# Kernel optimization log

Hardware: AMD Instinct MI355X
Metric: run time of the kernel (lower is better)

Reference implementation:

```python
import jax, jax.numpy as jnp
import numpy as np

B, N, C = 2, 2048, 1024
H = 16
D = C // H  # 64
EPS = 1e-6


def rms_norm(x, w):
    # LlamaRMSNorm: fp32 variance over last dim
    xf = x.astype(jnp.float32)
    var = jnp.mean(xf * xf, axis=-1, keepdims=True)
    xf = xf * jax.lax.rsqrt(var + EPS)
    return (w * xf).astype(x.dtype)


def setup_inputs() -> dict:
    key = jax.random.key(0)
    ks = jax.random.split(key, 4)
    x = jax.random.normal(ks[0], (B, N, C), dtype=jnp.float32)
    mask = jax.random.randint(ks[1], (B, N), 0, 2, dtype=jnp.int32)
    qkv_w = jax.random.normal(ks[2], (3 * C, C), dtype=jnp.float32) * (1.0 / np.sqrt(C))
    qkv_b = jnp.zeros((3 * C,), dtype=jnp.float32)
    proj_w = jax.random.normal(ks[3], (C, C), dtype=jnp.float32) * (1.0 / np.sqrt(C))
    proj_b = jnp.zeros((C,), dtype=jnp.float32)
    qn_w = jnp.ones((D,), dtype=jnp.float32)
    kn_w = jnp.ones((D,), dtype=jnp.float32)
    return {"x": x, "mask": mask, "qkv_w": qkv_w, "qkv_b": qkv_b,
            "proj_w": proj_w, "proj_b": proj_b, "qn_w": qn_w, "kn_w": kn_w}


def reference(x, mask, qkv_w, qkv_b, proj_w, proj_b, qn_w, kn_w):
    dtype = x.dtype
    scale = D ** -0.5
    # qkv projection -> (3, B, H, N, D)
    qkv = (x @ qkv_w.T + qkv_b).reshape(B, N, 3, H, D).transpose(2, 0, 3, 1, 4)
    q, k, v = qkv[0], qkv[1], qkv[2]
    q = rms_norm(q, qn_w)
    k = rms_norm(k, kn_w)
    q = q * scale
    # scores in fp32, key-padding mask [B,1,1,N]
    attn = jnp.einsum('bhnd,bhmd->bhnm', q, k).astype(jnp.float32)
    key_mask = (mask != 0)[:, None, None, :]
    attn = jnp.where(key_mask, attn, jnp.float32(-1e9))
    attn = jax.nn.softmax(attn, axis=-1).astype(dtype)
    out = jnp.einsum('bhnm,bhmd->bhnd', attn, v)  # (B,H,N,D)
    out = out.transpose(0, 2, 1, 3).reshape(B, N, C)
    return out @ proj_w.T + proj_b
```

## Files before the change

kernel.cpp:

```cpp
#include <hip/hip_runtime.h>
#include <hip/hip_bf16.h>
#include <stdint.h>

namespace {

constexpr int kB = 2;
constexpr int kN = 2048;
constexpr int kC = 1024;
constexpr int kH = 16;
constexpr int kD = 64;
constexpr int kTok = kB * kN;
constexpr int k3C  = 3 * kC;
constexpr size_t kPS = (size_t)kTok * k3C;
constexpr size_t kXE = (size_t)kTok * kC;
constexpr size_t kWQ = (size_t)k3C * kC;
constexpr size_t kWP = (size_t)kC * kC;

using bhalf8 = __attribute__((ext_vector_type(8))) __bf16;
using f32x4  = __attribute__((ext_vector_type(4))) float;

__device__ inline unsigned short f2bf(float f) {
  __hip_bfloat16 h = __float2bfloat16(f);
  return *reinterpret_cast<unsigned short*>(&h);
}
__device__ inline float bf2f(unsigned short u) {
  __hip_bfloat16 h;
  *reinterpret_cast<unsigned short*>(&h) = u;
  return __bfloat162float(h);
}
__device__ inline void split2(float v, unsigned short& h, unsigned short& l) {
  const unsigned short hb = f2bf(v);
  h = hb;
  l = f2bf(v - bf2f(hb));
}

__device__ inline void glds16(const unsigned short* g, unsigned short* l) {
  __builtin_amdgcn_global_load_lds(
      (const __attribute__((address_space(1))) void*)g,
      (__attribute__((address_space(3))) void*)l, 16, 0, 0);
}

__global__ __launch_bounds__(256)
void split_planes(const float* __restrict__ src,
                  unsigned short* __restrict__ H,
                  unsigned short* __restrict__ L, int n4)
{
  const int i = blockIdx.x * 256 + threadIdx.x;
  if (i >= n4) return;
  const float4 v = ((const float4*)src)[i];
  ushort4 hh, ll;
  split2(v.x, hh.x, ll.x); split2(v.y, hh.y, ll.y);
  split2(v.z, hh.z, ll.z); split2(v.w, hh.w, ll.w);
  ((ushort4*)H)[i] = hh;
  ((ushort4*)L)[i] = ll;
}

__global__ __launch_bounds__(256)
void vt_transpose(const unsigned short* __restrict__ H,
                  unsigned short* __restrict__ VTH)
{
  const int gw   = blockIdx.x * 4 + (threadIdx.x >> 6);
  const int lane = threadIdx.x & 63;
  const int bh   = gw >> 8;
  const int oct  = gw & 255;
  const int b = bh >> 4, h = bh & 15;
  const int tok0 = oct * 8;
  union { unsigned short u[8]; uint4 v; } ph;
  #pragma unroll
  for (int e = 0; e < 8; ++e) {
    const size_t g = (size_t)(b * kN + tok0 + e) * k3C + 2 * kC + h * kD + lane;
    ph.u[e] = H[g];
  }
  *(uint4*)(&VTH[((size_t)bh * kD + lane) * kN + tok0]) = ph.v;
}

__global__ __launch_bounds__(512)
void gemm_qkv256(const unsigned short* __restrict__ AH,
                 const unsigned short* __restrict__ AL,
                 const unsigned short* __restrict__ WH,
                 const unsigned short* __restrict__ WL,
                 const float* __restrict__ bias,
                 unsigned short* __restrict__ OutH,
                 unsigned short* __restrict__ OutL,
                 const float* __restrict__ qn,
                 const float* __restrict__ kn)
{
  constexpr int BK = 32;
  constexpr int NT = kC / BK;

  __shared__ __align__(16) unsigned short sA[2][2][256 * 32];
  __shared__ __align__(16) unsigned short sB[2][2][256 * 32];

  const int tt   = threadIdx.x;
  const int wave = tt >> 6;
  const int lane = tt & 63;
  const int quad = lane >> 4;
  const int l16  = lane & 15;
  const int bm = blockIdx.x * 256;
  const int bn = blockIdx.y * 256;
  const int wm = (wave >> 2) * 128;
  const int wn = (wave & 3) * 64;

  int srow[2], scol[2];
  #pragma unroll
  for (int r = 0; r < 2; ++r) {
    const int u = r * 512 + tt;
    srow[r] = u >> 2;
    scol[r] = ((u & 3) ^ ((srow[r] >> 1) & 3)) * 8;
  }

  auto stagePair = [&](int buf, int k0, int which) {
    const unsigned short* src = (which == 0) ? AH : (which == 1) ? AL
                              : (which == 2) ? WH : WL;
    const int base = (which < 2) ? bm : bn;
    unsigned short* dst = (which < 2) ? &sA[buf][which][0]
                                      : &sB[buf][which - 2][0];
    #pragma unroll
    for (int r = 0; r < 2; ++r) {
      glds16(&src[(size_t)(base + srow[r]) * kC + k0 + scol[r]],
             &dst[(r * 512 + tt) * 8]);
    }
  };

  f32x4 acc[8][4] = {};

  #pragma unroll
  for (int w = 0; w < 4; ++w) stagePair(0, 0, w);

  for (int t = 0; t < NT; ++t) {
    const int buf  = t & 1;
    const int nbuf = buf ^ 1;
    const int nk0  = (t + 1) * BK;
    bhalf8 bh_[4], bl_[4];

    #pragma unroll
    for (int p = 0; p < 4; ++p) {
      bhalf8 ah[2], al[2];
      if (p == 0) {
        if (t < NT - 1) {
          stagePair(nbuf, nk0, 0);
          asm volatile("s_waitcnt vmcnt(2)" ::: "memory");
        } else {
          asm volatile("s_waitcnt vmcnt(0)" ::: "memory");
        }
        __builtin_amdgcn_sched_barrier(0);
        asm volatile("s_barrier" ::: "memory");
        #pragma unroll
        for (int j = 0; j < 4; ++j) {
          const int row = wn + j * 16 + l16;
          const int off = row * 32 + ((quad ^ ((row >> 1) & 3)) * 8);
          bh_[j] = *(const bhalf8*)(&sB[buf][0][off]);
          bl_[j] = *(const bhalf8*)(&sB[buf][1][off]);
        }
        #pragma unroll
        for (int e = 0; e < 2; ++e) {
          const int row = wm + e * 16 + l16;
          const int off = row * 32 + ((quad ^ ((row >> 1) & 3)) * 8);
          ah[e] = *(const bhalf8*)(&sA[buf][0][off]);
          al[e] = *(const bhalf8*)(&sA[buf][1][off]);
        }
      } else {
        #pragma unroll
        for (int e = 0; e < 2; ++e) {
          const int row = wm + (2 * p + e) * 16 + l16;
          const int off = row * 32 + ((quad ^ ((row >> 1) & 3)) * 8);
          ah[e] = *(const bhalf8*)(&sA[buf][0][off]);
          al[e] = *(const bhalf8*)(&sA[buf][1][off]);
        }
        if (t < NT - 1) stagePair(nbuf, nk0, p);
        asm volatile("s_barrier" ::: "memory");
      }

      __builtin_amdgcn_s_setprio(1);
      #pragma unroll
      for (int e = 0; e < 2; ++e) {
        const int i = 2 * p + e;
        #pragma unroll
        for (int j = 0; j < 4; ++j) {
          f32x4 a = acc[i][j];
          a = __builtin_amdgcn_mfma_f32_16x16x32_bf16(ah[e], bh_[j], a, 0, 0, 0);
          a = __builtin_amdgcn_mfma_f32_16x16x32_bf16(ah[e], bl_[j], a, 0, 0, 0);
          a = __builtin_amdgcn_mfma_f32_16x16x32_bf16(al[e], bh_[j], a, 0, 0, 0);
          acc[i][j] = a;
        }
      }
      __builtin_amdgcn_s_setprio(0);
      asm volatile("s_barrier" ::: "memory");
    }
  }

  const int slice = bn >> 10;
  const bool writeL = (slice == 0);
  float bv[4], wv[4];
  #pragma unroll
  for (int j = 0; j < 4; ++j) {
    bv[j] = bias[bn + wn + j * 16 + l16];
    if (slice < 2) wv[j] = (slice ? kn : qn)[j * 16 + l16];
  }

  #pragma unroll
  for (int i = 0; i < 8; ++i) {
    float val[4][4];
    #pragma unroll
    for (int j = 0; j < 4; ++j)
      #pragma unroll
      for (int r = 0; r < 4; ++r)
        val[j][r] = acc[i][j][r] + bv[j];

    if (slice < 2) {
      #pragma unroll
      for (int r = 0; r < 4; ++r) {
        float ss = val[0][r] * val[0][r];
        #pragma unroll
        for (int j = 1; j < 4; ++j) ss += val[j][r] * val[j][r];
        #pragma unroll
        for (int d = 1; d < 16; d <<= 1) ss += __shfl_xor(ss, d, 64);
        float rinv = rsqrtf(ss * (1.0f / 64.0f) + 1e-6f);
        if (slice == 0) rinv *= 0.125f;
        #pragma unroll
        for (int j = 0; j < 4; ++j) val[j][r] = wv[j] * (val[j][r] * rinv);
      }
    }

    #pragma unroll
    for (int j = 0; j < 4; ++j) {
      const int n = bn + wn + j * 16 + l16;
      #pragma unroll
      for (int r = 0; r < 4; ++r) {
        const int m = bm + wm + i * 16 + quad * 4 + r;
        unsigned short hh, ll;
        split2(val[j][r], hh, ll);
        OutH[(size_t)m * k3C + n] = hh;
        if (writeL) OutL[(size_t)m * k3C + n] = ll;
      }
    }
  }
}

template<bool OUTF32, bool FUSE_NORM>
__global__ __launch_bounds__(256)
void gemm_planes(const unsigned short* __restrict__ AH,
                 const unsigned short* __restrict__ AL, int lda,
                 const unsigned short* __restrict__ WH,
                 const unsigned short* __restrict__ WL,
                 const float* __restrict__ bias,
                 float* __restrict__ OutF,
                 unsigned short* __restrict__ OutH,
                 unsigned short* __restrict__ OutL,
                 const float* __restrict__ qn,
                 const float* __restrict__ kn,
                 int Nn, int K)
{
  __shared__ __align__(16) unsigned short AsH[128 * 32], AsL[128 * 32];
  __shared__ __align__(16) unsigned short BsH[128 * 32], BsL[128 * 32];

  const int t    = threadIdx.x;
  const int wave = t >> 6;
  const int lane = t & 63;
  const int quad = lane >> 4;
  const int l16  = lane & 15;
  const int bm = blockIdx.x * 128;
  const int bn = blockIdx.y * 128;
  const int wm = (wave >> 1) * 64;
  const int wn = (wave & 1) * 64;

  f32x4 acc[4][4] = {};

  for (int k0 = 0; k0 < K; k0 += 32) {
    #pragma unroll
    for (int r = 0; r < 2; ++r) {
      const int c   = r * 256 + t;
      const int row = c >> 2;
      const int col = (c & 3) * 8;
      glds16(&AH[(size_t)(bm + row) * lda + k0 + col], &AsH[c * 8]);
      glds16(&AL[(size_t)(bm + row) * lda + k0 + col], &AsL[c * 8]);
      glds16(&WH[(size_t)(bn + row) * K + k0 + col], &BsH[c * 8]);
      glds16(&WL[(size_t)(bn + row) * K + k0 + col], &BsL[c * 8]);
    }
    __syncthreads();

    bhalf8 afh[4], afl[4], bgh[4], bgl[4];
    #pragma unroll
    for (int i = 0; i < 4; ++i) {
      afh[i] = *(const bhalf8*)(&AsH[(wm + i * 16 + l16) * 32 + quad * 8]);
      afl[i] = *(const bhalf8*)(&AsL[(wm + i * 16 + l16) * 32 + quad * 8]);
      bgh[i] = *(const bhalf8*)(&BsH[(wn + i * 16 + l16) * 32 + quad * 8]);
      bgl[i] = *(const bhalf8*)(&BsL[(wn + i * 16 + l16) * 32 + quad * 8]);
    }
    #pragma unroll
    for (int i = 0; i < 4; ++i)
      #pragma unroll
      for (int j = 0; j < 4; ++j) {
        f32x4 a = acc[i][j];
        a = __builtin_amdgcn_mfma_f32_16x16x32_bf16(afh[i], bgh[j], a, 0, 0, 0);
        a = __builtin_amdgcn_mfma_f32_16x16x32_bf16(afh[i], bgl[j], a, 0, 0, 0);
        a = __builtin_amdgcn_mfma_f32_16x16x32_bf16(afl[i], bgh[j], a, 0, 0, 0);
        acc[i][j] = a;
      }
    __syncthreads();
  }

  float bv[4], wv[4];
  const int slice = FUSE_NORM ? (bn >> 10) : 0;
  const bool writeL = !FUSE_NORM || slice == 0;
  #pragma unroll
  for (int j = 0; j < 4; ++j) {
    bv[j] = bias[bn + wn + j * 16 + l16];
    if (FUSE_NORM && slice < 2)
      wv[j] = (slice ? kn : qn)[j * 16 + l16];
  }

  #pragma unroll
  for (int i = 0; i < 4; ++i) {
    float val[4][4];
    #pragma unroll
    for (int j = 0; j < 4; ++j)
      #pragma unroll
      for (int r = 0; r < 4; ++r)
        val[j][r] = acc[i][j][r] + bv[j];

    if (FUSE_NORM && slice < 2) {
      #pragma unroll
      for (int r = 0; r < 4; ++r) {
        float ss = val[0][r] * val[0][r];
        #pragma unroll
        for (int j = 1; j < 4; ++j) ss += val[j][r] * val[j][r];
        #pragma unroll
        for (int d = 1; d < 16; d <<= 1) ss += __shfl_xor(ss, d, 64);
        float rinv = rsqrtf(ss * (1.0f / 64.0f) + 1e-6f);
        if (slice == 0) rinv *= 0.125f;
        #pragma unroll
        for (int j = 0; j < 4; ++j) val[j][r] = wv[j] * (val[j][r] * rinv);
      }
    }

    #pragma unroll
    for (int j = 0; j < 4; ++j) {
      const int n = bn + wn + j * 16 + l16;
      #pragma unroll
      for (int r = 0; r < 4; ++r) {
        const int m = bm + wm + i * 16 + quad * 4 + r;
        if (OUTF32) {
          OutF[(size_t)m * Nn + n] = val[j][r];
        } else {
          unsigned short hh, ll;
          split2(val[j][r], hh, ll);
          OutH[(size_t)m * Nn + n] = hh;
          if (writeL) OutL[(size_t)m * Nn + n] = ll;
        }
      }
    }
  }
}

__global__ __launch_bounds__(256)
void attn_kernel(unsigned short* __restrict__ H, unsigned short* __restrict__ L,
                 const unsigned short* __restrict__ VTH,
                 const int* __restrict__ mask)
{
  constexpr int P = 72;
  __shared__ __align__(16) unsigned short KtH[64 * P];
  __shared__ __align__(16) unsigned short VtH[64 * P];
  __shared__ __align__(16) unsigned short Pt[4][32 * P];

  const int t    = threadIdx.x;
  const int wave = t >> 6;
  const int lane = t & 63;
  const int quad = lane >> 4;
  const int l16  = lane & 15;

  const int lin  = blockIdx.x;
  const int xcd  = lin & 7;
  const int slot = lin >> 3;
  const int bh   = xcd + 8 * (slot >> 4);
  const int qblk = slot & 15;
  const int b  = bh >> 4;
  const int h  = bh & 15;
  const int q0 = qblk * 128 + wave * 32;

  const int row0 = t >> 3,         col0 = (t & 7) * 8;
  const int row1 = (256 + t) >> 3, col1 = ((256 + t) & 7) * 8;

  bhalf8 qfh[2][2], qfl[2][2];
  #pragma unroll
  for (int g = 0; g < 2; ++g) {
    const size_t qrow = (size_t)(b * kN + q0 + g * 16 + l16) * k3C + h * kD;
    qfh[g][0] = *(const bhalf8*)(&H[qrow + quad * 8]);
    qfh[g][1] = *(const bhalf8*)(&H[qrow + 32 + quad * 8]);
    qfl[g][0] = *(const bhalf8*)(&L[qrow + quad * 8]);
    qfl[g][1] = *(const bhalf8*)(&L[qrow + 32 + quad * 8]);
  }

  f32x4 acc_o[2][4] = {};
  float lpart[2][4] = {};

  uint4 sk0, sk1, sv0, sv1;
  int mcur[4], mnext[4];

  auto pref = [&](int kt) {
    sk0 = *(const uint4*)(&H[(size_t)(b * kN + kt + row0) * k3C + kC + h * kD + col0]);
    sk1 = *(const uint4*)(&H[(size_t)(b * kN + kt + row1) * k3C + kC + h * kD + col1]);
    sv0 = *(const uint4*)(&VTH[((size_t)bh * kD + row0) * kN + kt + col0]);
    sv1 = *(const uint4*)(&VTH[((size_t)bh * kD + row1) * kN + kt + col1]);
  };
  auto loadM = [&](int kt, int* m) {
    #pragma unroll
    for (int nt = 0; nt < 4; ++nt) m[nt] = mask[b * kN + kt + nt * 16 + l16];
  };

  pref(0);
  loadM(0, mcur);

  for (int i = 0; i < 32; ++i) {
    const int kt = i * 64;
    *(uint4*)(&KtH[row0 * P + col0]) = sk0;
    *(uint4*)(&KtH[row1 * P + col1]) = sk1;
    *(uint4*)(&VtH[row0 * P + col0]) = sv0;
    *(uint4*)(&VtH[row1 * P + col1]) = sv1;
    __syncthreads();

    if (i < 31) { pref(kt + 64); loadM(kt + 64, mnext); }

    #pragma unroll
    for (int nt = 0; nt < 4; ++nt) {
      const int kr = (nt * 16 + l16) * P + quad * 8;
      const bhalf8 kh0 = *(const bhalf8*)(&KtH[kr]);
      const bhalf8 kh1 = *(const bhalf8*)(&KtH[kr + 32]);
      const float flag = mcur[nt] ? 1.0f : 0.0f;
      #pragma unroll
      for (int g = 0; g < 2; ++g) {
        f32x4 s = {};
        s = __builtin_amdgcn_mfma_f32_16x16x32_bf16(qfh[g][0], kh0, s, 0, 0, 0);
        s = __builtin_amdgcn_mfma_f32_16x16x32_bf16(qfh[g][1], kh1, s, 0, 0, 0);
        s = __builtin_amdgcn_mfma_f32_16x16x32_bf16(qfl[g][0], kh0, s, 0, 0, 0);
        s = __builtin_amdgcn_mfma_f32_16x16x32_bf16(qfl[g][1], kh1, s, 0, 0, 0);
        #pragma unroll
        for (int r = 0; r < 4; ++r) {
          const float p = flag * __expf(s[r]);
          lpart[g][r] += p;
          Pt[wave][(g * 16 + quad * 4 + r) * P + nt * 16 + l16] = f2bf(p);
        }
      }
    }

    #pragma unroll
    for (int kk = 0; kk < 2; ++kk) {
      const bhalf8 pa0 = *(const bhalf8*)(&Pt[wave][l16 * P + kk * 32 + quad * 8]);
      const bhalf8 pa1 = *(const bhalf8*)(&Pt[wave][(16 + l16) * P + kk * 32 + quad * 8]);
      #pragma unroll
      for (int dt = 0; dt < 4; ++dt) {
        const bhalf8 vb = *(const bhalf8*)(&VtH[(dt * 16 + l16) * P + kk * 32 + quad * 8]);
        acc_o[0][dt] = __builtin_amdgcn_mfma_f32_16x16x32_bf16(pa0, vb, acc_o[0][dt], 0, 0, 0);
        acc_o[1][dt] = __builtin_amdgcn_mfma_f32_16x16x32_bf16(pa1, vb, acc_o[1][dt], 0, 0, 0);
      }
    }

    #pragma unroll
    for (int nt = 0; nt < 4; ++nt) mcur[nt] = mnext[nt];
    __syncthreads();
  }

  #pragma unroll
  for (int g = 0; g < 2; ++g)
    #pragma unroll
    for (int r = 0; r < 4; ++r) {
      float s = lpart[g][r];
      #pragma unroll
      for (int d = 1; d < 16; d <<= 1) s += __shfl_xor(s, d, 64);
      lpart[g][r] = s;
    }
  #pragma unroll
  for (int g = 0; g < 2; ++g)
    #pragma unroll
    for (int dt = 0; dt < 4; ++dt)
      #pragma unroll
      for (int r = 0; r < 4; ++r) {
        const int qrow = q0 + g * 16 + quad * 4 + r;
        const float inv = 1.0f / fmaxf(lpart[g][r], 1.0e-30f);
        const size_t off = (size_t)(b * kN + qrow) * k3C + h * kD + dt * 16 + l16;
        unsigned short hh, ll;
        split2(acc_o[g][dt][r] * inv, hh, ll);
        H[off] = hh; L[off] = ll;
      }
}

}

extern "C" void kernel_launch(void* const* d_in, const int* in_sizes, int n_in,
                              void* d_out, int out_size, void* d_ws, size_t ws_size,
                              hipStream_t stream)
{
  const float* x      = (const float*)d_in[0];
  const int*   maskp  = (const int*)d_in[1];
  const float* qkv_w  = (const float*)d_in[2];
  const float* qkv_b  = (const float*)d_in[3];
  const float* proj_w = (const float*)d_in[4];
  const float* proj_b = (const float*)d_in[5];
  const float* qn_w   = (const float*)d_in[6];
  const float* kn_w   = (const float*)d_in[7];
  float* out = (float*)d_out;

  unsigned short* qH = (unsigned short*)d_ws;
  unsigned short* qL = qH + kPS;
  unsigned short* R1 = qL + kPS;
  unsigned short* R2 = R1 + 2 * kXE;
  unsigned short* xH = R1,  *xL = R1 + kXE;
  unsigned short* VTH = R1;
  unsigned short* wqH = R2, *wqL = R2 + kWQ;
  unsigned short* wpH = R2, *wpL = R2 + kWP;

  split_planes<<<(int)(kXE / 4 / 256), 256, 0, stream>>>(x, xH, xL, (int)(kXE / 4));
  split_planes<<<(int)(kWQ / 4 / 256), 256, 0, stream>>>(qkv_w, wqH, wqL, (int)(kWQ / 4));

  gemm_qkv256<<<dim3(kTok / 256, k3C / 256), 512, 0, stream>>>(
      xH, xL, wqH, wqL, qkv_b, qH, qL, qn_w, kn_w);

  vt_transpose<<<2048, 256, 0, stream>>>(qH, VTH);
  split_planes<<<(int)(kWP / 4 / 256), 256, 0, stream>>>(proj_w, wpH, wpL, (int)(kWP / 4));

  attn_kernel<<<dim3(512), 256, 0, stream>>>(qH, qL, VTH, maskp);

  gemm_planes<true, false><<<dim3(kTok / 128, kC / 128), 256, 0, stream>>>(
      qH, qL, k3C, wpH, wpL, proj_b, out, nullptr, nullptr, nullptr, nullptr, kC, kC);
}
```

Baseline: 311.4 us.

## Restructure split-bf16 GEMM main loop into plane-ordered phases with finer-grained staging

Reorganizes the QKV GEMM inner loop so each k-tile is processed as three phases (AH*WH, AH*WL, AL*WH), loading the LDS planes in the order they are consumed. Global-to-LDS staging for the next tile is interleaved per plane with partial vmcnt waits, and the last iteration is peeled. The aim is better overlap of memory traffic with MFMA work and fewer barriers per tile. In exchange it keeps more fragments live in registers (8 A fragments), which may raise register pressure and lower occupancy.

```diff
diff --git a/kernel.cpp b/kernel.cpp
--- a/kernel.cpp
+++ b/kernel.cpp
@@ -109,84 +109,147 @@
     scol[r] = ((u & 3) ^ ((srow[r] >> 1) & 3)) * 8;
   }
 
-  auto stagePair = [&](int buf, int k0, int which) {
-    const unsigned short* src = (which == 0) ? AH : (which == 1) ? AL
-                              : (which == 2) ? WH : WL;
-    const int base = (which < 2) ? bm : bn;
-    unsigned short* dst = (which < 2) ? &sA[buf][which][0]
-                                      : &sB[buf][which - 2][0];
-    #pragma unroll
-    for (int r = 0; r < 2; ++r) {
+  auto stageU = [&](int bf, int k0, int which) {
+    const unsigned short* src = (which == 0) ? AH : (which == 1) ? WH
+                              : (which == 2) ? WL : AL;
+    const int base = (which == 0 || which == 3) ? bm : bn;
+    unsigned short* dst = (which == 0) ? &sA[bf][0][0]
+                        : (which == 3) ? &sA[bf][1][0]
+                        : (which == 1) ? &sB[bf][0][0] : &sB[bf][1][0];
+    #pragma unroll
+    for (int r = 0; r < 2; ++r)
       glds16(&src[(size_t)(base + srow[r]) * kC + k0 + scol[r]],
              &dst[(r * 512 + tt) * 8]);
-    }
   };
 
+  auto rdA = [&](int bf, int pl, int row) -> bhalf8 {
+    return *(const bhalf8*)(&sA[bf][pl][row * 32 + ((quad ^ ((row >> 1) & 3)) * 8)]);
+  };
+  auto rdB = [&](int bf, int pl, int row) -> bhalf8 {
+    return *(const bhalf8*)(&sB[bf][pl][row * 32 + ((quad ^ ((row >> 1) & 3)) * 8)]);
+  };
+
   f32x4 acc[8][4] = {};
-
-  #pragma unroll
-  for (int w = 0; w < 4; ++w) stagePair(0, 0, w);
-
-  for (int t = 0; t < NT; ++t) {
+  bhalf8 ah[8], bh_[4], bl_[4];
+
+  stageU(0, 0, 0); stageU(0, 0, 1); stageU(0, 0, 2); stageU(0, 0, 3);
+  asm volatile("s_waitcnt vmcnt(4)" ::: "memory");
+  __builtin_amdgcn_sched_barrier(0);
+  asm volatile("s_barrier" ::: "memory");
+
+  for (int t = 0; t < NT - 1; ++t) {
     const int buf  = t & 1;
     const int nbuf = buf ^ 1;
     const int nk0  = (t + 1) * BK;
-    bhalf8 bh_[4], bl_[4];
-
-    #pragma unroll
-    for (int p = 0; p < 4; ++p) {
-      bhalf8 ah[2], al[2];
-      if (p == 0) {
-        if (t < NT - 1) {
-          stagePair(nbuf, nk0, 0);
-          asm volatile("s_waitcnt vmcnt(2)" ::: "memory");
-        } else {
-          asm volatile("s_waitcnt vmcnt(0)" ::: "memory");
-        }
-        __builtin_amdgcn_sched_barrier(0);
-        asm volatile("s_barrier" ::: "memory");
-        #pragma unroll
-        for (int j = 0; j < 4; ++j) {
-          const int row = wn + j * 16 + l16;
-          const int off = row * 32 + ((quad ^ ((row >> 1) & 3)) * 8);
-          bh_[j] = *(const bhalf8*)(&sB[buf][0][off]);
-          bl_[j] = *(const bhalf8*)(&sB[buf][1][off]);
-        }
-        #pragma unroll
-        for (int e = 0; e < 2; ++e) {
-          const int row = wm + e * 16 + l16;
-          const int off = row * 32 + ((quad ^ ((row >> 1) & 3)) * 8);
-          ah[e] = *(const bhalf8*)(&sA[buf][0][off]);
-          al[e] = *(const bhalf8*)(&sA[buf][1][off]);
-        }
-      } else {
-        #pragma unroll
-        for (int e = 0; e < 2; ++e) {
-          const int row = wm + (2 * p + e) * 16 + l16;
-          const int off = row * 32 + ((quad ^ ((row >> 1) & 3)) * 8);
-          ah[e] = *(const bhalf8*)(&sA[buf][0][off]);
-          al[e] = *(const bhalf8*)(&sA[buf][1][off]);
-        }
-        if (t < NT - 1) stagePair(nbuf, nk0, p);
-        asm volatile("s_barrier" ::: "memory");
-      }
-
-      __builtin_amdgcn_s_setprio(1);
-      #pragma unroll
-      for (int e = 0; e < 2; ++e) {
-        const int i = 2 * p + e;
-        #pragma unroll
-        for (int j = 0; j < 4; ++j) {
-          f32x4 a = acc[i][j];
-          a = __builtin_amdgcn_mfma_f32_16x16x32_bf16(ah[e], bh_[j], a, 0, 0, 0);
-          a = __builtin_amdgcn_mfma_f32_16x16x32_bf16(ah[e], bl_[j], a, 0, 0, 0);
-          a = __builtin_amdgcn_mfma_f32_16x16x32_bf16(al[e], bh_[j], a, 0, 0, 0);
-          acc[i][j] = a;
-        }
-      }
-      __builtin_amdgcn_s_setprio(0);
-      asm volatile("s_barrier" ::: "memory");
-    }
+
+    #pragma unroll
+    for (int i = 0; i < 8; ++i) ah[i]  = rdA(buf, 0, wm + i * 16 + l16);
+    #pragma unroll
+    for (int j = 0; j < 4; ++j) bh_[j] = rdB(buf, 0, wn + j * 16 + l16);
+    stageU(nbuf, nk0, 0);
+    stageU(nbuf, nk0, 1);
+    asm volatile("s_waitcnt vmcnt(6)" ::: "memory");
+    __builtin_amdgcn_sched_barrier(0);
+    asm volatile("s_barrier" ::: "memory");
+    __builtin_amdgcn_s_setprio(1);
+    #pragma unroll
+    for (int i = 0; i < 8; ++i)
+      #pragma unroll
+      for (int j = 0; j < 4; ++j)
+        acc[i][j] = __builtin_amdgcn_mfma_f32_16x16x32_bf16(ah[i], bh_[j], acc[i][j], 0, 0, 0);
+    __builtin_amdgcn_s_setprio(0);
+
+    #pragma unroll
+    for (int j = 0; j < 4; ++j) bl_[j] = rdB(buf, 1, wn + j * 16 + l16);
+    stageU(nbuf, nk0, 2);
+    asm volatile("s_waitcnt vmcnt(6)" ::: "memory");
+    __builtin_amdgcn_sched_barrier(0);
+    asm volatile("s_barrier" ::: "memory");
+    __builtin_amdgcn_s_setprio(1);
+    #pragma unroll
+    for (int i = 0; i < 8; ++i)
+      #pragma unroll
+      for (int j = 0; j < 4; ++j)
+        acc[i][j] = __builtin_amdgcn_mfma_f32_16x16x32_bf16(ah[i], bl_[j], acc[i][j], 0, 0, 0);
+    __builtin_amdgcn_s_setprio(0);
+
+    stageU(nbuf, nk0, 3);
+    asm volatile("s_waitcnt vmcnt(4)" ::: "memory");
+    __builtin_amdgcn_sched_barrier(0);
+    asm volatile("s_barrier" ::: "memory");
+    __builtin_amdgcn_s_setprio(1);
+    {
+      bhalf8 al0[4];
+      #pragma unroll
+      for (int i = 0; i < 4; ++i) al0[i] = rdA(buf, 1, wm + i * 16 + l16);
+      #pragma unroll
+      for (int i = 0; i < 4; ++i)
+        #pragma unroll
+        for (int j = 0; j < 4; ++j)
+          acc[i][j] = __builtin_amdgcn_mfma_f32_16x16x32_bf16(al0[i], bh_[j], acc[i][j], 0, 0, 0);
+      bhalf8 al1[4];
+      #pragma unroll
+      for (int i = 0; i < 4; ++i) al1[i] = rdA(buf, 1, wm + (4 + i) * 16 + l16);
+      #pragma unroll
+      for (int i = 0; i < 4; ++i)
+        #pragma unroll
+        for (int j = 0; j < 4; ++j)
+          acc[4 + i][j] = __builtin_amdgcn_mfma_f32_16x16x32_bf16(al1[i], bh_[j], acc[4 + i][j], 0, 0, 0);
+    }
+    __builtin_amdgcn_s_setprio(0);
+    asm volatile("s_barrier" ::: "memory");
+  }
+
+  {
+    const int buf = (NT - 1) & 1;
+    #pragma unroll
+    for (int i = 0; i < 8; ++i) ah[i]  = rdA(buf, 0, wm + i * 16 + l16);
+    #pragma unroll
+    for (int j = 0; j < 4; ++j) bh_[j] = rdB(buf, 0, wn + j * 16 + l16);
+    __builtin_amdgcn_s_setprio(1);
+    #pragma unroll
+    for (int i = 0; i < 8; ++i)
+      #pragma unroll
+      for (int j = 0; j < 4; ++j)
+        acc[i][j] = __builtin_amdgcn_mfma_f32_16x16x32_bf16(ah[i], bh_[j], acc[i][j], 0, 0, 0);
+    __builtin_amdgcn_s_setprio(0);
+
+    asm volatile("s_waitcnt vmcnt(2)" ::: "memory");
+    __builtin_amdgcn_sched_barrier(0);
+    asm volatile("s_barrier" ::: "memory");
+    #pragma unroll
+    for (int j = 0; j < 4; ++j) bl_[j] = rdB(buf, 1, wn + j * 16 + l16);
+    __builtin_amdgcn_s_setprio(1);
+    #pragma unroll
+    for (int i = 0; i < 8; ++i)
+      #pragma unroll
+      for (int j = 0; j < 4; ++j)
+        acc[i][j] = __builtin_amdgcn_mfma_f32_16x16x32_bf16(ah[i], bl_[j], acc[i][j], 0, 0, 0);
+    __builtin_amdgcn_s_setprio(0);
+
+    asm volatile("s_waitcnt vmcnt(0)" ::: "memory");
+    __builtin_amdgcn_sched_barrier(0);
+    asm volatile("s_barrier" ::: "memory");
+    __builtin_amdgcn_s_setprio(1);
+    {
+      bhalf8 al0[4];
+      #pragma unroll
+      for (int i = 0; i < 4; ++i) al0[i] = rdA(buf, 1, wm + i * 16 + l16);
+      #pragma unroll
+      for (int i = 0; i < 4; ++i)
+        #pragma unroll
+        for (int j = 0; j < 4; ++j)
+          acc[i][j] = __builtin_amdgcn_mfma_f32_16x16x32_bf16(al0[i], bh_[j], acc[i][j], 0, 0, 0);
+      bhalf8 al1[4];
+      #pragma unroll
+      for (int i = 0; i < 4; ++i) al1[i] = rdA(buf, 1, wm + (4 + i) * 16 + l16);
+      #pragma unroll
+      for (int i = 0; i < 4; ++i)
+        #pragma unroll
+        for (int j = 0; j < 4; ++j)
+          acc[4 + i][j] = __builtin_amdgcn_mfma_f32_16x16x32_bf16(al1[i], bh_[j], acc[4 + i][j], 0, 0, 0);
+    }
+    __builtin_amdgcn_s_setprio(0);
   }
 
   const int slice = bn >> 10;
```

Result: faster. 299.7 us (-3.8%).
